# Kernel tuning notes

Hardware: AMD Instinct MI355X
Metric: run time of the kernel (lower is better)

Reference implementation:

```python
import jax, jax.numpy as jnp
import numpy as np

KSIZE = 20      # gaussian smoothing kernel size
SIGMA = 2.0     # gaussianSmoothWidth
STRIDE = 4      # strideLen
KLEN = 14       # kernelLen
LN_EPS = 1e-5


def _gauss_smooth(x):
    # x: [B, T, D]; depthwise conv1d along time, padding='same' (torch: left 9, right 10)
    D = x.shape[-1]
    i = jnp.arange(KSIZE, dtype=x.dtype)
    g = jnp.exp(-0.5 * ((i - (KSIZE - 1) / 2.0) / SIGMA) ** 2)
    g = g / jnp.sum(g)
    k = jnp.tile(g[None, None, :], (D, 1, 1))  # [D, 1, KSIZE]
    y = jax.lax.conv_general_dilated(
        jnp.swapaxes(x, 1, 2), k,
        window_strides=(1,), padding=[(9, 10)],
        feature_group_count=D,
        dimension_numbers=('NCW', 'OIW', 'NCW'))
    return jnp.swapaxes(y, 1, 2)


def _qrnn_layer(x, W, b):
    # SpeechBrain QuasiRNNLayer (output_gate=True, unidirectional, zoneout=0)
    # x: [B, T, F]; W: [3H, 2F]; b: [3H]
    xprev = jnp.concatenate([jnp.zeros_like(x[:, :1]), x[:, :-1]], axis=1)
    y = jnp.einsum('btf,gf->btg', jnp.concatenate([x, xprev], axis=-1), W) + b
    z, f, o = jnp.split(y, 3, axis=-1)
    z = jnp.tanh(z)
    f = jax.nn.sigmoid(f)
    fz = f * z
    # recurrence: c_t = f_t*z_t + (1-f_t)*c_{t-1}, c_0-input = 0
    def step(c, ins):
        f_t, fz_t = ins
        c = fz_t + (1.0 - f_t) * c
        return c, c
    c0 = jnp.zeros((f.shape[0], f.shape[2]), f.dtype)
    _, cs = jax.lax.scan(step, c0, (jnp.swapaxes(f, 0, 1), jnp.swapaxes(fz, 0, 1)))
    c = jnp.swapaxes(cs, 0, 1)  # [B, T, H]
    return jax.nn.sigmoid(o) * c


def reference(neuralInput, dayWeights, dayBias, w0, b0, w_rest, b_rest,
              ln_gamma, ln_beta, w_out, b_out, dayIdx):
    x = _gauss_smooth(neuralInput)                    # [B, T, D]
    Wd = dayWeights[dayIdx]                           # [B, D, D]
    bd = dayBias[dayIdx]                              # [B, 1, D]
    x = jnp.einsum('btd,bdk->btk', x, Wd) + bd
    x = x / (1.0 + jnp.abs(x))                        # Softsign
    B, T, D = x.shape
    Tp = (T - KLEN) // STRIDE + 1
    idx = jnp.arange(Tp)[:, None] * STRIDE + jnp.arange(KLEN)[None, :]
    win = x[:, idx, :]                                # [B, Tp, K, D]
    # torch Unfold ordering: channel-major -> feature index = d*KLEN + k
    strided = jnp.transpose(win, (0, 1, 3, 2)).reshape(B, Tp, D * KLEN)
    h = _qrnn_layer(strided, w0, b0)
    for i in range(w_rest.shape[0]):
        h = _qrnn_layer(h, w_rest[i], b_rest[i])
    mu = jnp.mean(h, axis=-1, keepdims=True)
    var = jnp.mean(jnp.square(h - mu), axis=-1, keepdims=True)
    hn = (h - mu) * jax.lax.rsqrt(var + LN_EPS) * ln_gamma + ln_beta
    return jnp.einsum('bth,ch->btc', hn, w_out) + b_out


def setup_inputs() -> dict:
    key = jax.random.key(0)
    ks = jax.random.split(key, 10)
    B, T, D, H, L, NDAYS, C = 32, 2000, 256, 512, 3, 24, 41
    F0 = D * KLEN  # 3584
    inp = {}
    inp['neuralInput'] = jax.random.normal(ks[0], (B, T, D), jnp.float32)
    inp['dayIdx'] = jax.random.randint(ks[1], (B,), 0, NDAYS, jnp.int64 if jax.config.jax_enable_x64 else jnp.int32)
    eye = jnp.eye(D, dtype=jnp.float32)
    inp['dayWeights'] = eye[None] + 0.02 * jax.random.normal(ks[2], (NDAYS, D, D), jnp.float32)
    inp['dayBias'] = jnp.zeros((NDAYS, 1, D), jnp.float32)
    inp['w0'] = jax.random.normal(ks[3], (3 * H, 2 * F0), jnp.float32) / np.sqrt(2 * F0)
    inp['b0'] = jnp.zeros((3 * H,), jnp.float32)
    inp['w_rest'] = jax.random.normal(ks[4], (L - 1, 3 * H, 2 * H), jnp.float32) / np.sqrt(2 * H)
    inp['b_rest'] = jnp.zeros((L - 1, 3 * H), jnp.float32)
    inp['ln_gamma'] = jnp.ones((H,), jnp.float32)
    inp['ln_beta'] = jnp.zeros((H,), jnp.float32)
    inp['w_out'] = jax.random.normal(ks[5], (C, H), jnp.float32) / np.sqrt(H)
    inp['b_out'] = jnp.zeros((C,), jnp.float32)
    return inp
```

## Files before the change

### kernel.cpp

```cpp
#include <hip/hip_runtime.h>
#include <hip/hip_bf16.h>

typedef __hip_bfloat16 bf16;
typedef __attribute__((ext_vector_type(8))) short bf16x8;
typedef __attribute__((ext_vector_type(4))) float f32x4;

__device__ __forceinline__ float fsig(float x) { return 1.f / (1.f + __expf(-x)); }
__device__ __forceinline__ float ftanh(float x) { return 1.f - 2.f / (1.f + __expf(2.f * x)); }

#define GT 16
__global__ __launch_bounds__(256) void gauss_kernel(const float* __restrict__ X,
                                                    bf16* __restrict__ Y, int T) {
  int b = blockIdx.y, t0 = blockIdx.x * GT;
  int tid = threadIdx.x;
  __shared__ float xs[GT + 19][256];
  const float* xb = X + (long)b * T * 256;
  for (int r = 0; r < GT + 19; ++r) {
    int tt = t0 + r - 9;
    xs[r][tid] = (tt >= 0 && tt < T) ? xb[(long)tt * 256 + tid] : 0.f;
  }
  __syncthreads();
  float g[20];
  float norm = 0.f;
#pragma unroll
  for (int j = 0; j < 20; ++j) {
    float u = (j - 9.5f) * 0.5f;
    g[j] = expf(-0.5f * u * u);
    norm += g[j];
  }
  float rn = 1.f / norm;
  for (int i = 0; i < GT; ++i) {
    int t = t0 + i;
    if (t >= T) break;
    float acc = 0.f;
#pragma unroll
    for (int j = 0; j < 20; ++j) acc += g[j] * xs[i + j][tid];
    Y[((long)b * T + t) * 256 + tid] = (bf16)(acc * rn);
  }
}

__global__ __launch_bounds__(256) void transpose_day(const float* __restrict__ W,
                                                     bf16* __restrict__ Wt) {
  __shared__ float tile[64][65];
  int d0 = blockIdx.x * 64, g0 = blockIdx.y * 64, day = blockIdx.z;
  const float* Wd = W + (long)day * 65536;
  int tx = threadIdx.x & 63, ty = threadIdx.x >> 6;
  for (int i = 0; i < 16; ++i) {
    int d = ty + i * 4;
    tile[d][tx] = Wd[(long)(d0 + d) * 256 + g0 + tx];
  }
  __syncthreads();
  bf16* outp = Wt + (((long)day * 4 + (d0 >> 6)) * 256 + g0) * 64;
  for (int i = 0; i < 16; ++i) {
    int g = ty + i * 4;
    outp[(long)g * 64 + tx] = (bf16)tile[tx][g];
  }
}

__global__ void prep_misc(const float* __restrict__ w0, const float* __restrict__ w_rest,
                          bf16* __restrict__ V2, bf16* __restrict__ wrb2,
                          bf16* __restrict__ w0b, bf16* __restrict__ h1s,
                          bf16* __restrict__ h2s, bf16* __restrict__ zpage) {
  long i = (long)blockIdx.x * 256 + threadIdx.x;
  if (i < 7077888L) {
    int u = (int)(i / (1536 * 256));
    int r = (int)(i % (1536 * 256));
    int g = r >> 8, d = r & 255;
    float v = 0.f;
    if (u < 14) v += w0[(long)g * 7168 + 3584 + d * 14 + u];
    if (u >= 4) v += w0[(long)g * 7168 + d * 14 + (u - 4)];
    V2[(((long)u * 4 + (d >> 6)) * 1536 + g) * 64 + (d & 63)] = (bf16)v;
    return;
  }
  i -= 7077888L;
  if (i < 3145728L) {
    int L = (int)(i / (1536 * 1024));
    int r = (int)(i % (1536 * 1024));
    int g = r >> 10, k = r & 1023;
    float v = w_rest[(long)L * 1536 * 1024 + (long)g * 1024 + (k ^ 512)];
    wrb2[(long)L * 16 * 1536 * 64 + ((long)(k >> 6) * 1536 + g) * 64 + (k & 63)] = (bf16)v;
    return;
  }
  i -= 3145728L;
  if (i < 5505024L) {
    long g = i / 3584;
    int j = (int)(i - g * 3584);
    w0b[i] = (bf16)w0[g * 7168 + j];
    return;
  }
  i -= 5505024L;
  if (i < 16384) {
    int b = (int)(i >> 9), k = (int)(i & 511);
    h1s[(long)b * 498 * 512 + k] = (bf16)0.f;
    h2s[(long)b * 498 * 512 + k] = (bf16)0.f;
    return;
  }
  i -= 16384;
  if (i < 128) zpage[i] = (bf16)0.f;
}

__global__ __launch_bounds__(256, 4) void mfma97(
    const bf16* __restrict__ A, const bf16* __restrict__ W,
    const float* __restrict__ bias, bf16* __restrict__ Y,
    const int* __restrict__ dayIdx, const bf16* __restrict__ zpage,
    long astride, int Ta, int rstride, int Tm, int N, int tstride,
    int ntaps, int nch, int tap_off0, int NW, long dayWStride,
    int dayBStride, int mode, int nti, int ngi) {
  __shared__ __align__(16) char smem[32768];
  const int id = blockIdx.x;
  const int bi = id / (ngi * nti);
  const int rem = id - bi * (ngi * nti);
  const int gi = rem / nti;
  const int ti = rem - gi * nti;
  const int g0 = gi * 128, t0 = ti * 128;

  const bf16* Ab = A + (long)bi * astride;
  long wbase = 0;
  int boff = 0;
  if (dayIdx) {
    int di = dayIdx[bi];
    wbase = (long)di * dayWStride;
    boff = di * dayBStride;
  }
  const int tid = threadIdx.x;
  const int lane = tid & 63;
  const int w = tid >> 6;
  const int wm = (w >> 1) * 64, wn = (w & 1) * 64;
  const int lr = lane & 15, lg = lane >> 4;

  f32x4 acc[4][4] = {};

  for (int tap = 0; tap < ntaps; ++tap) {
    for (int dblk = 0; dblk < nch; ++dblk) {
      int d0 = dblk << 6;
      int s = tap * nch + dblk;
      const bf16* Wp = W + wbase + ((long)s * NW + g0) * 64;
#pragma unroll
      for (int j = 0; j < 8; ++j) {
        int q = j * 256 + tid;
        int qw = j * 256 + w * 64;
        const bf16* src;
        if (j < 4) {
          int row = q >> 3;
          int u = (q & 7) ^ (row & 7);
          int time = (t0 + row) * tstride + tap + tap_off0;
          src = (time >= 0 && time < Ta) ? Ab + (long)time * rstride + d0 + u * 8
                                         : zpage;
        } else {
          int row = (q >> 3) - 128;
          int u = (q & 7) ^ (row & 7);
          src = Wp + row * 64 + u * 8;
        }
        auto lp = (__attribute__((address_space(3))) void*)(smem + qw * 16);
        __builtin_amdgcn_global_load_lds(
            (const __attribute__((address_space(1))) void*)src, lp, 16, 0, 0);
      }
      __syncthreads();
#pragma unroll
      for (int kc = 0; kc < 2; ++kc) {
        int ub = kc * 4 + lg;
        bf16x8 af[4], bw[4];
#pragma unroll
        for (int f = 0; f < 4; ++f) {
          int m = wm + f * 16 + lr;
          af[f] = *reinterpret_cast<const bf16x8*>(smem + m * 128 + ((ub ^ (m & 7)) << 4));
          int g = wn + f * 16 + lr;
          bw[f] = *reinterpret_cast<const bf16x8*>(smem + 16384 + g * 128 +
                                                   ((ub ^ (g & 7)) << 4));
        }
#pragma unroll
        for (int fm = 0; fm < 4; ++fm)
#pragma unroll
          for (int fn = 0; fn < 4; ++fn)
            acc[fm][fn] = __builtin_amdgcn_mfma_f32_16x16x32_bf16(af[fm], bw[fn],
                                                                  acc[fm][fn], 0, 0, 0);
      }
      __syncthreads();
    }
  }
#pragma unroll
  for (int fn = 0; fn < 4; ++fn) {
    int gcol = g0 + wn + fn * 16 + lr;
    float bb = bias[boff + gcol];
    int sect = gcol >> 9;
#pragma unroll
    for (int fm = 0; fm < 4; ++fm) {
#pragma unroll
      for (int rr = 0; rr < 4; ++rr) {
        int t = t0 + wm + fm * 16 + lg * 4 + rr;
        if (t >= Tm) continue;
        float v = acc[fm][fn][rr] + bb;
        float e;
        if (mode == 1) e = v / (1.f + fabsf(v));
        else e = (sect == 0) ? ftanh(v) : fsig(v);
        Y[((long)bi * Tm + t) * N + gcol] = (bf16)e;
      }
    }
  }
}

__global__ void build_A0(const bf16* __restrict__ xs, bf16* __restrict__ A0) {
  int idx = blockIdx.x * 256 + threadIdx.x;
  if (idx >= 32 * 3584) return;
  int b = idx / 3584, j = idx % 3584;
  int d = j / 14, u = j % 14;
  A0[idx] = xs[((long)b * 2000 + u) * 256 + d];
}

__global__ __launch_bounds__(256) void t0_gemm(const bf16* __restrict__ A0,
                                               const bf16* __restrict__ W0b,
                                               float* __restrict__ part) {
  int g0 = blockIdx.x * 128;
  int ks = blockIdx.y;
  int k0 = ks * 512;
  __shared__ __align__(16) bf16 Wl[128 * 64];
  __shared__ __align__(16) bf16 Alds[32 * 64];
  int tid = threadIdx.x;
  int lane = tid & 63, wave = tid >> 6;
  int wn = wave * 32;
  int lr = lane & 15, lg = lane >> 4;
  int srow = tid >> 3, su = tid & 7;
  f32x4 acc[2][2] = {};
  for (int c = 0; c < 8; ++c) {
    int d0 = k0 + c * 64;
#pragma unroll
    for (int i = 0; i < 4; ++i) {
      int m = srow + i * 32;
      *reinterpret_cast<bf16x8*>(&Wl[m * 64 + ((su ^ (m & 7)) << 3)]) =
          *reinterpret_cast<const bf16x8*>(W0b + (long)(g0 + m) * 3584 + d0 + su * 8);
    }
    {
      int m = srow;
      *reinterpret_cast<bf16x8*>(&Alds[m * 64 + ((su ^ (m & 7)) << 3)]) =
          *reinterpret_cast<const bf16x8*>(A0 + (long)m * 3584 + d0 + su * 8);
    }
    __syncthreads();
#pragma unroll
    for (int kc = 0; kc < 2; ++kc) {
      int ub = kc * 4 + lg;
      bf16x8 am[2], bw[2];
#pragma unroll
      for (int f = 0; f < 2; ++f) {
        int m = f * 16 + lr;
        am[f] = *reinterpret_cast<const bf16x8*>(&Alds[m * 64 + ((ub ^ (m & 7)) << 3)]);
        int g = wn + f * 16 + lr;
        bw[f] = *reinterpret_cast<const bf16x8*>(&Wl[g * 64 + ((ub ^ (g & 7)) << 3)]);
      }
#pragma unroll
      for (int fm = 0; fm < 2; ++fm)
#pragma unroll
        for (int fn = 0; fn < 2; ++fn)
          acc[fm][fn] = __builtin_amdgcn_mfma_f32_16x16x32_bf16(am[fm], bw[fn],
                                                                acc[fm][fn], 0, 0, 0);
    }
    __syncthreads();
  }
#pragma unroll
  for (int fn = 0; fn < 2; ++fn) {
    int gcol = g0 + wn + fn * 16 + lr;
#pragma unroll
    for (int fm = 0; fm < 2; ++fm)
#pragma unroll
      for (int r = 0; r < 4; ++r) {
        int brow = fm * 16 + lg * 4 + r;
        part[((long)ks * 32 + brow) * 1536 + gcol] = acc[fm][fn][r];
      }
  }
}

__global__ void t0_reduce(const float* __restrict__ part, const float* __restrict__ b0,
                          bf16* __restrict__ yact, int Tp) {
  int idx = blockIdx.x * 256 + threadIdx.x;
  if (idx >= 32 * 1536) return;
  int b = idx / 1536, g = idx % 1536;
  float s = b0[g];
#pragma unroll
  for (int k = 0; k < 7; ++k) s += part[((long)k * 32 + b) * 1536 + g];
  float e = (g < 512) ? ftanh(s) : fsig(s);
  yact[(long)b * Tp * 1536 + g] = (bf16)e;
}

#define NC 8
#define LC 63
__global__ __launch_bounds__(256) void scan_pass1(const bf16* __restrict__ Yv,
                                                  float* __restrict__ Afac,
                                                  float* __restrict__ Bfac, int Tp) {
  int idx = blockIdx.x * 256 + threadIdx.x;
  int ci = idx >> 14;
  int chain = idx & 16383;
  int b = chain >> 9, hh = chain & 511;
  const bf16* yb = Yv + (long)b * Tp * 1536 + hh;
  int t0 = ci * LC, t1 = min(t0 + LC, Tp);
  float A = 1.f, Bv = 0.f;
  for (int t = t0; t < t1; ++t) {
    const bf16* p = yb + (long)t * 1536;
    float zt = (float)p[0], fs = (float)p[512];
    Bv = fs * zt + (1.f - fs) * Bv;
    A *= (1.f - fs);
  }
  Afac[idx] = A;
  Bfac[idx] = Bv;
}

__global__ void scan_pass2(const float* __restrict__ Afac, const float* __restrict__ Bfac,
                           float* __restrict__ cst) {
  int chain = blockIdx.x * 256 + threadIdx.x;
  float c = 0.f;
#pragma unroll
  for (int ci = 0; ci < NC; ++ci) {
    cst[ci * 16384 + chain] = c;
    c = Afac[ci * 16384 + chain] * c + Bfac[ci * 16384 + chain];
  }
}

__global__ __launch_bounds__(256) void scan_pass3(const bf16* __restrict__ Yv,
                                                  const float* __restrict__ cst,
                                                  bf16* __restrict__ H, int Tp) {
  int idx = blockIdx.x * 256 + threadIdx.x;
  int ci = idx >> 14;
  int chain = idx & 16383;
  int b = chain >> 9, hh = chain & 511;
  const bf16* yb = Yv + (long)b * Tp * 1536 + hh;
  bf16* hb = H + ((long)b * 498 + 1) * 512 + hh;
  int t0 = ci * LC, t1 = min(t0 + LC, Tp);
  float c = cst[ci * 16384 + chain];
  for (int t = t0; t < t1; ++t) {
    const bf16* p = yb + (long)t * 1536;
    float zt = (float)p[0], fs = (float)p[512], so = (float)p[1024];
    c = fs * zt + (1.f - fs) * c;
    hb[(long)t * 512] = (bf16)(so * c);
  }
}

__global__ __launch_bounds__(256) void ln_out_kernel(
    const bf16* __restrict__ Hs, const float* __restrict__ gamma,
    const float* __restrict__ beta, const float* __restrict__ Wo,
    const float* __restrict__ bo, float* __restrict__ Out) {
  long bt = blockIdx.x;
  int b = (int)(bt / 497), t = (int)(bt % 497);
  const bf16* hrow = Hs + ((long)b * 498 + 1 + t) * 512;
  int tid = threadIdx.x;
  float v0 = (float)hrow[tid], v1 = (float)hrow[tid + 256];
  float s = v0 + v1, s2 = v0 * v0 + v1 * v1;
#pragma unroll
  for (int d = 32; d; d >>= 1) {
    s += __shfl_down(s, d);
    s2 += __shfl_down(s2, d);
  }
  __shared__ float rs[4], rs2[4];
  int wid = tid >> 6, lane = tid & 63;
  if (lane == 0) {
    rs[wid] = s;
    rs2[wid] = s2;
  }
  __syncthreads();
  float sum = rs[0] + rs[1] + rs[2] + rs[3];
  float sum2 = rs2[0] + rs2[1] + rs2[2] + rs2[3];
  float mu = sum * (1.f / 512.f);
  float var = sum2 * (1.f / 512.f) - mu * mu;
  float rstd = rsqrtf(var + 1e-5f);
  __shared__ float hl[512];
  hl[tid] = (v0 - mu) * rstd * gamma[tid] + beta[tid];
  hl[tid + 256] = (v1 - mu) * rstd * gamma[tid + 256] + beta[tid + 256];
  __syncthreads();
  const float4* hp = reinterpret_cast<const float4*>(&hl[lane * 8]);
  float4 h0v = hp[0], h1v = hp[1];
  for (int c = wid; c < 41; c += 4) {
    const float4* wp = reinterpret_cast<const float4*>(Wo + (long)c * 512 + lane * 8);
    float4 w0v = wp[0], w1v = wp[1];
    float a = w0v.x * h0v.x + w0v.y * h0v.y + w0v.z * h0v.z + w0v.w * h0v.w +
              w1v.x * h1v.x + w1v.y * h1v.y + w1v.z * h1v.z + w1v.w * h1v.w;
#pragma unroll
    for (int d = 32; d; d >>= 1) a += __shfl_down(a, d);
    if (lane == 0) Out[bt * 41 + c] = a + bo[c];
  }
}

extern "C" void kernel_launch(void* const* d_in, const int* in_sizes, int n_in,
                              void* d_out, int out_size, void* d_ws, size_t ws_size,
                              hipStream_t stream) {
  const float* neuralInput = (const float*)d_in[0];
  const int* dayIdx = (const int*)d_in[1];
  const float* dayWeights = (const float*)d_in[2];
  const float* dayBias = (const float*)d_in[3];
  const float* w0 = (const float*)d_in[4];
  const float* b0 = (const float*)d_in[5];
  const float* w_rest = (const float*)d_in[6];
  const float* b_rest = (const float*)d_in[7];
  const float* ln_gamma = (const float*)d_in[8];
  const float* ln_beta = (const float*)d_in[9];
  const float* w_out = (const float*)d_in[10];
  const float* b_out = (const float*)d_in[11];
  float* out = (float*)d_out;

  const int B = 32, T = 2000, Tp = 497;

  char* p = (char*)d_ws;
  bf16* yact = (bf16*)p;  p += 48857088;
  bf16* xs0b = (bf16*)p;  p += 32768000;
  bf16* xs = (bf16*)p;    p += 32768000;
  bf16* V2 = (bf16*)p;    p += 14155776;
  bf16* dWb2 = (bf16*)p;  p += 3145728;
  bf16* wrb2 = (bf16*)p;  p += 6291456;
  bf16* w0b = (bf16*)p;   p += 11010048;
  bf16* A0 = (bf16*)p;    p += 229376;
  float* part = (float*)p; p += 1376256;
  bf16* h1s = (bf16*)p;   p += 16320512;
  bf16* h2s = (bf16*)p;   p += 16320512;
  float* Afac = (float*)p; p += 524288;
  float* Bfac = (float*)p; p += 524288;
  float* cst = (float*)p;  p += 524288;
  bf16* zpage = (bf16*)p;  p += 256;

  hipLaunchKernelGGL(prep_misc, dim3((15745152L + 255) / 256), dim3(256), 0, stream,
                     w0, w_rest, V2, wrb2, w0b, h1s, h2s, zpage);
  hipLaunchKernelGGL(transpose_day, dim3(4, 4, 24), dim3(256), 0, stream, dayWeights, dWb2);
  hipLaunchKernelGGL(gauss_kernel, dim3((T + GT - 1) / GT, B), dim3(256), 0, stream,
                     neuralInput, xs0b, T);
  hipLaunchKernelGGL(mfma97, dim3(1024), dim3(256), 0, stream, xs0b, dWb2, dayBias,
                     xs, dayIdx, zpage, (long)T * 256, T, 256, T, 256, 1, 1, 4, 0,
                     256, 65536L, 256, 1, 16, 2);
  hipLaunchKernelGGL(build_A0, dim3((32 * 3584 + 255) / 256), dim3(256), 0, stream, xs, A0);
  hipLaunchKernelGGL(t0_gemm, dim3(12, 7), dim3(256), 0, stream, A0, w0b, part);
  hipLaunchKernelGGL(mfma97, dim3(1536), dim3(256), 0, stream, xs, V2, b0, yact,
                     (const int*)nullptr, zpage, (long)T * 256, T, 256, Tp, 1536, 4,
                     18, 4, -4, 1536, 0L, 0, 2, 4, 12);
  hipLaunchKernelGGL(t0_reduce, dim3((32 * 1536 + 255) / 256), dim3(256), 0, stream,
                     part, b0, yact, Tp);
  hipLaunchKernelGGL(scan_pass1, dim3(512), dim3(256), 0, stream, yact, Afac, Bfac, Tp);
  hipLaunchKernelGGL(scan_pass2, dim3(64), dim3(256), 0, stream, Afac, Bfac, cst);
  hipLaunchKernelGGL(scan_pass3, dim3(512), dim3(256), 0, stream, yact, cst, h1s, Tp);
  for (int i = 0; i < 2; ++i) {
    bf16* hin = (i == 0) ? h1s : h2s;
    bf16* hout = (i == 0) ? h2s : h1s;
    hipLaunchKernelGGL(mfma97, dim3(1536), dim3(256), 0, stream, hin,
                       wrb2 + (long)i * 16 * 1536 * 64, b_rest + (long)i * 1536, yact,
                       (const int*)nullptr, zpage, 498L * 512, Tp, 512, Tp, 1536, 1,
                       1, 16, 0, 1536, 0L, 0, 2, 4, 12);
    hipLaunchKernelGGL(scan_pass1, dim3(512), dim3(256), 0, stream, yact, Afac, Bfac, Tp);
    hipLaunchKernelGGL(scan_pass2, dim3(64), dim3(256), 0, stream, Afac, Bfac, cst);
    hipLaunchKernelGGL(scan_pass3, dim3(512), dim3(256), 0, stream, yact, cst, hout, Tp);
  }
  hipLaunchKernelGGL(ln_out_kernel, dim3(B * Tp), dim3(256), 0, stream, h1s,
                     ln_gamma, ln_beta, w_out, b_out, out);
}
```

Measured before the change: 816.9 us.

## Replace 128x128 GEMM with 256x256 8-wave ping-pong pipelined kernel

Result: slower. 982.0 us (+20.2%).

```diff
diff --git a/kernel.cpp b/kernel.cpp
--- a/kernel.cpp
+++ b/kernel.cpp
@@ -99,101 +99,145 @@
   if (i < 128) zpage[i] = (bf16)0.f;
 }
 
-__global__ __launch_bounds__(256, 4) void mfma97(
+#define MMAC(ACC)                                                                   \
+  __builtin_amdgcn_s_setprio(1);                                                    \
+  _Pragma("unroll") for (int fm = 0; fm < 4; ++fm)                                  \
+      _Pragma("unroll") for (int fn = 0; fn < 4; ++fn)                              \
+          ACC[fm][fn] = __builtin_amdgcn_mfma_f32_16x16x32_bf16(af[fm], bw[fn],     \
+                                                                ACC[fm][fn], 0, 0, 0); \
+  __builtin_amdgcn_s_setprio(0);
+#define BAR __builtin_amdgcn_s_barrier()
+
+__global__ __launch_bounds__(512, 1) void gemm8ph(
     const bf16* __restrict__ A, const bf16* __restrict__ W,
     const float* __restrict__ bias, bf16* __restrict__ Y,
     const int* __restrict__ dayIdx, const bf16* __restrict__ zpage,
     long astride, int Ta, int rstride, int Tm, int N, int tstride,
     int ntaps, int nch, int tap_off0, int NW, long dayWStride,
-    int dayBStride, int mode, int nti, int ngi) {
-  __shared__ __align__(16) char smem[32768];
-  const int id = blockIdx.x;
-  const int bi = id / (ngi * nti);
-  const int rem = id - bi * (ngi * nti);
-  const int gi = rem / nti;
-  const int ti = rem - gi * nti;
-  const int g0 = gi * 128, t0 = ti * 128;
-
-  const bf16* Ab = A + (long)bi * astride;
+    int dayBStride, int mode, int nti) {
+  extern __shared__ char smem[];
+  const int nwg = gridDim.x;
+  const int id = (blockIdx.x & 7) * (nwg >> 3) + (blockIdx.x >> 3);
+  const int b = id & 31;
+  const int rem = id >> 5;
+  const int ti = rem % nti, gi = rem / nti;
+  const int g0 = gi * 256, t0 = ti * 256;
+
+  const bf16* Ab = A + (long)b * astride;
   long wbase = 0;
   int boff = 0;
   if (dayIdx) {
-    int di = dayIdx[bi];
+    int di = dayIdx[b];
     wbase = (long)di * dayWStride;
     boff = di * dayBStride;
   }
   const int tid = threadIdx.x;
   const int lane = tid & 63;
   const int w = tid >> 6;
-  const int wm = (w >> 1) * 64, wn = (w & 1) * 64;
+  const int wr = w >> 2, wc = w & 3;
   const int lr = lane & 15, lg = lane >> 4;
-
-  f32x4 acc[4][4] = {};
-
-  for (int tap = 0; tap < ntaps; ++tap) {
-    for (int dblk = 0; dblk < nch; ++dblk) {
-      int d0 = dblk << 6;
-      int s = tap * nch + dblk;
-      const bf16* Wp = W + wbase + ((long)s * NW + g0) * 64;
-#pragma unroll
-      for (int j = 0; j < 8; ++j) {
-        int q = j * 256 + tid;
-        int qw = j * 256 + w * 64;
-        const bf16* src;
-        if (j < 4) {
-          int row = q >> 3;
-          int u = (q & 7) ^ (row & 7);
-          int time = (t0 + row) * tstride + tap + tap_off0;
-          src = (time >= 0 && time < Ta) ? Ab + (long)time * rstride + d0 + u * 8
-                                         : zpage;
-        } else {
-          int row = (q >> 3) - 128;
-          int u = (q & 7) ^ (row & 7);
-          src = Wp + row * 64 + u * 8;
-        }
-        auto lp = (__attribute__((address_space(3))) void*)(smem + qw * 16);
-        __builtin_amdgcn_global_load_lds(
-            (const __attribute__((address_space(1))) void*)src, lp, 16, 0, 0);
+  const int ns = ntaps * nch;
+  const int niter = ns >> 1;
+
+  auto stage = [&](int p, int op, int c, int kt) {
+    int tap = kt / nch;
+    int d0 = (kt - tap * nch) << 6;
+    int base = p * 65536 + op * 32768 + c * 16384;
+    const bf16* Wp = W + wbase + ((long)kt * NW + g0) * 64 + c * 32;
+#pragma unroll
+    for (int j = 0; j < 2; ++j) {
+      int q = j * 512 + tid;
+      int row = q >> 2, u = q & 3;
+      const bf16* src;
+      if (op == 0) {
+        int time = (t0 + row) * tstride + tap + tap_off0;
+        src = (time >= 0 && time < Ta)
+                  ? Ab + (long)time * rstride + d0 + c * 32 + u * 8
+                  : zpage;
+      } else {
+        src = Wp + (long)row * 64 + u * 8;
       }
-      __syncthreads();
-#pragma unroll
-      for (int kc = 0; kc < 2; ++kc) {
-        int ub = kc * 4 + lg;
-        bf16x8 af[4], bw[4];
-#pragma unroll
-        for (int f = 0; f < 4; ++f) {
-          int m = wm + f * 16 + lr;
-          af[f] = *reinterpret_cast<const bf16x8*>(smem + m * 128 + ((ub ^ (m & 7)) << 4));
-          int g = wn + f * 16 + lr;
-          bw[f] = *reinterpret_cast<const bf16x8*>(smem + 16384 + g * 128 +
-                                                   ((ub ^ (g & 7)) << 4));
-        }
-#pragma unroll
-        for (int fm = 0; fm < 4; ++fm)
-#pragma unroll
-          for (int fn = 0; fn < 4; ++fn)
-            acc[fm][fn] = __builtin_amdgcn_mfma_f32_16x16x32_bf16(af[fm], bw[fn],
-                                                                  acc[fm][fn], 0, 0, 0);
-      }
-      __syncthreads();
-    }
-  }
+      auto lp = (__attribute__((address_space(3))) void*)(smem + base + (j * 512 + w * 64) * 16);
+      __builtin_amdgcn_global_load_lds(
+          (const __attribute__((address_space(1))) void*)src, lp, 16, 0, 0);
+    }
+  };
+
+  f32x4 accL[4][4] = {};
+  f32x4 accH[4][4] = {};
+  bf16x8 af[4], bw[4];
+
+  auto rdA = [&](int p, int c, int mh) {
+#pragma unroll
+    for (int f = 0; f < 4; ++f) {
+      int m = wr * 128 + mh * 64 + f * 16 + lr;
+      af[f] = *reinterpret_cast<const bf16x8*>(smem + p * 65536 + c * 16384 + m * 64 + lg * 16);
+    }
+  };
+  auto rdB = [&](int p, int c) {
+#pragma unroll
+    for (int f = 0; f < 4; ++f) {
+      int g = wc * 64 + f * 16 + lr;
+      bw[f] = *reinterpret_cast<const bf16x8*>(smem + p * 65536 + 32768 + c * 16384 + g * 64 + lg * 16);
+    }
+  };
+
+  stage(0, 0, 0, 0); stage(0, 1, 0, 0);
+  stage(0, 0, 1, 0); stage(0, 1, 1, 0);
+  stage(1, 0, 0, 1); stage(1, 1, 0, 1);
+  asm volatile("s_waitcnt vmcnt(8)" ::: "memory");
+  BAR;
+
+  for (int i = 0; i < niter; ++i) {
+    const int k0 = 2 * i, k1 = 2 * i + 1;
+    const bool more = (i + 1 < niter);
+    rdB(0, 0); rdA(0, 0, 0); stage(1, 0, 1, k1);
+    BAR; MMAC(accL); BAR;
+    rdA(0, 0, 1); stage(1, 1, 1, k1);
+    BAR; MMAC(accH);
+    if (more) { asm volatile("s_waitcnt vmcnt(8)" ::: "memory"); }
+    else      { asm volatile("s_waitcnt vmcnt(0)" ::: "memory"); }
+    BAR;
+    rdB(0, 1); rdA(0, 1, 0); if (more) stage(0, 0, 0, k0 + 2);
+    BAR; MMAC(accL); BAR;
+    rdA(0, 1, 1); if (more) stage(0, 1, 0, k0 + 2);
+    BAR; MMAC(accH);
+    if (more) { asm volatile("s_waitcnt vmcnt(8)" ::: "memory"); }
+    else      { asm volatile("s_waitcnt vmcnt(0)" ::: "memory"); }
+    BAR;
+    rdB(1, 0); rdA(1, 0, 0); if (more) stage(0, 0, 1, k0 + 2);
+    BAR; MMAC(accL); BAR;
+    rdA(1, 0, 1); if (more) stage(0, 1, 1, k0 + 2);
+    BAR; MMAC(accH);
+    if (more) { asm volatile("s_waitcnt vmcnt(8)" ::: "memory"); }
+    else      { asm volatile("s_waitcnt vmcnt(0)" ::: "memory"); }
+    BAR;
+    rdB(1, 1); rdA(1, 1, 0); if (more) stage(1, 0, 0, k1 + 2);
+    BAR; MMAC(accL); BAR;
+    rdA(1, 1, 1); if (more) stage(1, 1, 0, k1 + 2);
+    BAR; MMAC(accH);
+    if (more) { asm volatile("s_waitcnt vmcnt(8)" ::: "memory"); }
+    else      { asm volatile("s_waitcnt vmcnt(0)" ::: "memory"); }
+    BAR;
+  }
+
 #pragma unroll
   for (int fn = 0; fn < 4; ++fn) {
-    int gcol = g0 + wn + fn * 16 + lr;
+    int gcol = g0 + wc * 64 + fn * 16 + lr;
     float bb = bias[boff + gcol];
     int sect = gcol >> 9;
 #pragma unroll
-    for (int fm = 0; fm < 4; ++fm) {
+    for (int fm = 0; fm < 8; ++fm) {
+      f32x4 a = (fm < 4) ? accL[fm][fn] : accH[fm - 4][fn];
 #pragma unroll
       for (int rr = 0; rr < 4; ++rr) {
-        int t = t0 + wm + fm * 16 + lg * 4 + rr;
+        int t = t0 + wr * 128 + fm * 16 + lg * 4 + rr;
         if (t >= Tm) continue;
-        float v = acc[fm][fn][rr] + bb;
+        float v = a[rr] + bb;
         float e;
         if (mode == 1) e = v / (1.f + fabsf(v));
         else e = (sect == 0) ? ftanh(v) : fsig(v);
-        Y[((long)bi * Tm + t) * N + gcol] = (bf16)e;
+        Y[((long)b * Tm + t) * N + gcol] = (bf16)e;
       }
     }
   }
@@ -238,19 +282,19 @@
 #pragma unroll
     for (int kc = 0; kc < 2; ++kc) {
       int ub = kc * 4 + lg;
-      bf16x8 am[2], bw[2];
+      bf16x8 am[2], bwv[2];
 #pragma unroll
       for (int f = 0; f < 2; ++f) {
         int m = f * 16 + lr;
         am[f] = *reinterpret_cast<const bf16x8*>(&Alds[m * 64 + ((ub ^ (m & 7)) << 3)]);
         int g = wn + f * 16 + lr;
-        bw[f] = *reinterpret_cast<const bf16x8*>(&Wl[g * 64 + ((ub ^ (g & 7)) << 3)]);
+        bwv[f] = *reinterpret_cast<const bf16x8*>(&Wl[g * 64 + ((ub ^ (g & 7)) << 3)]);
       }
 #pragma unroll
       for (int fm = 0; fm < 2; ++fm)
 #pragma unroll
         for (int fn = 0; fn < 2; ++fn)
-          acc[fm][fn] = __builtin_amdgcn_mfma_f32_16x16x32_bf16(am[fm], bw[fn],
+          acc[fm][fn] = __builtin_amdgcn_mfma_f32_16x16x32_bf16(am[fm], bwv[fn],
                                                                 acc[fm][fn], 0, 0, 0);
     }
     __syncthreads();
@@ -412,19 +456,23 @@
   float* cst = (float*)p;  p += 524288;
   bf16* zpage = (bf16*)p;  p += 256;
 
+  const int LDS8 = 131072;
+  hipFuncSetAttribute(reinterpret_cast<const void*>(gemm8ph),
+                      hipFuncAttributeMaxDynamicSharedMemorySize, LDS8);
+
   hipLaunchKernelGGL(prep_misc, dim3((15745152L + 255) / 256), dim3(256), 0, stream,
                      w0, w_rest, V2, wrb2, w0b, h1s, h2s, zpage);
   hipLaunchKernelGGL(transpose_day, dim3(4, 4, 24), dim3(256), 0, stream, dayWeights, dWb2);
   hipLaunchKernelGGL(gauss_kernel, dim3((T + GT - 1) / GT, B), dim3(256), 0, stream,
                      neuralInput, xs0b, T);
-  hipLaunchKernelGGL(mfma97, dim3(1024), dim3(256), 0, stream, xs0b, dWb2, dayBias,
+  hipLaunchKernelGGL(gemm8ph, dim3(256), dim3(512), LDS8, stream, xs0b, dWb2, dayBias,
                      xs, dayIdx, zpage, (long)T * 256, T, 256, T, 256, 1, 1, 4, 0,
-                     256, 65536L, 256, 1, 16, 2);
+                     256, 65536L, 256, 1, 8);
   hipLaunchKernelGGL(build_A0, dim3((32 * 3584 + 255) / 256), dim3(256), 0, stream, xs, A0);
   hipLaunchKernelGGL(t0_gemm, dim3(12, 7), dim3(256), 0, stream, A0, w0b, part);
-  hipLaunchKernelGGL(mfma97, dim3(1536), dim3(256), 0, stream, xs, V2, b0, yact,
+  hipLaunchKernelGGL(gemm8ph, dim3(384), dim3(512), LDS8, stream, xs, V2, b0, yact,
                      (const int*)nullptr, zpage, (long)T * 256, T, 256, Tp, 1536, 4,
-                     18, 4, -4, 1536, 0L, 0, 2, 4, 12);
+                     18, 4, -4, 1536, 0L, 0, 2, 2);
   hipLaunchKernelGGL(t0_reduce, dim3((32 * 1536 + 255) / 256), dim3(256), 0, stream,
                      part, b0, yact, Tp);
   hipLaunchKernelGGL(scan_pass1, dim3(512), dim3(256), 0, stream, yact, Afac, Bfac, Tp);
@@ -433,10 +481,10 @@
   for (int i = 0; i < 2; ++i) {
     bf16* hin = (i == 0) ? h1s : h2s;
     bf16* hout = (i == 0) ? h2s : h1s;
-    hipLaunchKernelGGL(mfma97, dim3(1536), dim3(256), 0, stream, hin,
+    hipLaunchKernelGGL(gemm8ph, dim3(384), dim3(512), LDS8, stream, hin,
                        wrb2 + (long)i * 16 * 1536 * 64, b_rest + (long)i * 1536, yact,
                        (const int*)nullptr, zpage, 498L * 512, Tp, 512, Tp, 1536, 1,
-                       1, 16, 0, 1536, 0L, 0, 2, 4, 12);
+                       1, 16, 0, 1536, 0L, 0, 2, 2);
     hipLaunchKernelGGL(scan_pass1, dim3(512), dim3(256), 0, stream, yact, Afac, Bfac, Tp);
     hipLaunchKernelGGL(scan_pass2, dim3(64), dim3(256), 0, stream, Afac, Bfac, cst);
     hipLaunchKernelGGL(scan_pass3, dim3(512), dim3(256), 0, stream, yact, cst, hout, Tp);
```

## Add 256x256 ping-pong GEMM with direct-to-LDS loads and fold scan pass2 into pass3

Applied to the files above, without the earlier changes.

Measured after the change: 992.5 us. 21.5% more time.

```diff
diff --git a/kernel.cpp b/kernel.cpp
--- a/kernel.cpp
+++ b/kernel.cpp
@@ -97,6 +97,138 @@
   }
   i -= 16384;
   if (i < 128) zpage[i] = (bf16)0.f;
+}
+
+#define MM16(MH)                                                                     \
+  __builtin_amdgcn_s_setprio(1);                                                     \
+  _Pragma("unroll") for (int fm = 0; fm < 4; ++fm)                                   \
+      _Pragma("unroll") for (int fn = 0; fn < 4; ++fn)                               \
+          acc[MH][fm][fn] = __builtin_amdgcn_mfma_f32_16x16x32_bf16(                 \
+              af[fm], bw[fn], acc[MH][fm][fn], 0, 0, 0);                             \
+  __builtin_amdgcn_s_setprio(0);
+#define BAR __builtin_amdgcn_s_barrier()
+
+__global__ __launch_bounds__(512, 1) void gemm8p2(
+    const bf16* __restrict__ A, const bf16* __restrict__ W,
+    const float* __restrict__ bias, bf16* __restrict__ Y,
+    const bf16* __restrict__ zpage, long astride, int Ta, int rstride,
+    int Tm, int N, int tstride, int ntaps, int nch, int tap_off0, int NW,
+    int nti) {
+  extern __shared__ char smem[];
+  const int nwg = gridDim.x;
+  const int id = (blockIdx.x & 7) * (nwg >> 3) + (blockIdx.x >> 3);
+  const int ngi = N >> 8;
+  const int per_b = ngi * nti;
+  const int b = id / per_b;
+  const int rem = id - b * per_b;
+  const int gi = rem / nti, ti = rem - (rem / nti) * nti;
+  const int g0 = gi * 256, t0 = ti * 256;
+
+  const bf16* Ab = A + (long)b * astride;
+  const int tid = threadIdx.x;
+  const int lane = tid & 63;
+  const int w = tid >> 6;
+  const int wr = w >> 2, wc = w & 3;
+  const int lr = lane & 15, lg = lane >> 4;
+  const int ns = ntaps * nch;
+  const int niter = ns >> 1;
+
+  auto st = [&](int p, int op, int h, int kt) {
+    int tap = kt / nch;
+    int d0 = (kt - tap * nch) << 6;
+    int base = p * 65536 + op * 32768 + h * 16384;
+#pragma unroll
+    for (int j = 0; j < 2; ++j) {
+      int q = j * 512 + tid;
+      int row = h * 128 + (q >> 3);
+      int u = (q & 7) ^ (row & 7);
+      const bf16* src;
+      if (op == 0) {
+        int time = (t0 + row) * tstride + tap + tap_off0;
+        src = (time >= 0 && time < Ta) ? Ab + (long)time * rstride + d0 + u * 8
+                                       : zpage;
+      } else {
+        src = W + ((long)kt * NW + g0 + row) * 64 + u * 8;
+      }
+      auto lp = (__attribute__((address_space(3))) void*)(smem + base + (j * 512 + w * 64) * 16);
+      __builtin_amdgcn_global_load_lds(
+          (const __attribute__((address_space(1))) void*)src, lp, 16, 0, 0);
+    }
+  };
+
+  f32x4 acc[2][4][4] = {};
+  bf16x8 af[4], bw[4];
+
+  auto rdA = [&](int p, int c, int mh) {
+#pragma unroll
+    for (int f = 0; f < 4; ++f) {
+      int m = wr * 128 + mh * 64 + f * 16 + lr;
+      af[f] = *reinterpret_cast<const bf16x8*>(
+          smem + p * 65536 + m * 128 + (((c * 4 + lg) ^ (m & 7)) << 4));
+    }
+  };
+  auto rdB = [&](int p, int c) {
+#pragma unroll
+    for (int f = 0; f < 4; ++f) {
+      int g = wc * 64 + f * 16 + lr;
+      bw[f] = *reinterpret_cast<const bf16x8*>(
+          smem + p * 65536 + 32768 + g * 128 + (((c * 4 + lg) ^ (g & 7)) << 4));
+    }
+  };
+
+  st(0, 0, 0, 0); st(0, 0, 1, 0); st(0, 1, 0, 0); st(0, 1, 1, 0);
+  st(1, 0, 0, 1);
+  asm volatile("s_waitcnt vmcnt(2)" ::: "memory");
+  BAR;
+
+#pragma unroll 1
+  for (int i = 0; i < niter; ++i) {
+    const int k0 = 2 * i, k1 = 2 * i + 1;
+    const bool more = (i + 1 < niter);
+    rdA(0, 0, 0); rdB(0, 0); st(1, 0, 1, k1);
+    BAR; MM16(0); BAR;
+    rdA(0, 0, 1); st(1, 1, 0, k1);
+    BAR; MM16(1); BAR;
+    rdA(0, 1, 0); rdB(0, 1); st(1, 1, 1, k1);
+    BAR; MM16(0); BAR;
+    rdA(0, 1, 1); if (more) st(0, 0, 0, k0 + 2);
+    BAR; MM16(1);
+    if (more) { asm volatile("s_waitcnt vmcnt(2)" ::: "memory"); }
+    else      { asm volatile("s_waitcnt vmcnt(0)" ::: "memory"); }
+    BAR;
+    rdA(1, 0, 0); rdB(1, 0); if (more) st(0, 0, 1, k0 + 2);
+    BAR; MM16(0); BAR;
+    rdA(1, 0, 1); if (more) st(0, 1, 0, k0 + 2);
+    BAR; MM16(1); BAR;
+    rdA(1, 1, 0); rdB(1, 1); if (more) st(0, 1, 1, k0 + 2);
+    BAR; MM16(0); BAR;
+    rdA(1, 1, 1); if (more) st(1, 0, 0, k1 + 2);
+    BAR; MM16(1);
+    if (more) { asm volatile("s_waitcnt vmcnt(2)" ::: "memory"); }
+    else      { asm volatile("s_waitcnt vmcnt(0)" ::: "memory"); }
+    BAR;
+  }
+
+#pragma unroll
+  for (int fn = 0; fn < 4; ++fn) {
+    int gcol = g0 + wc * 64 + fn * 16 + lr;
+    float bb = bias[gcol];
+    int sect = gcol >> 9;
+#pragma unroll
+    for (int mh = 0; mh < 2; ++mh) {
+#pragma unroll
+      for (int fm = 0; fm < 4; ++fm) {
+#pragma unroll
+        for (int rr = 0; rr < 4; ++rr) {
+          int t = t0 + wr * 128 + mh * 64 + fm * 16 + lg * 4 + rr;
+          if (t >= Tm) continue;
+          float v = acc[mh][fm][fn][rr] + bb;
+          float e = (sect == 0) ? ftanh(v) : fsig(v);
+          Y[((long)b * Tm + t) * N + gcol] = (bf16)e;
+        }
+      }
+    }
+  }
 }
 
 __global__ __launch_bounds__(256, 4) void mfma97(
@@ -238,19 +370,19 @@
 #pragma unroll
     for (int kc = 0; kc < 2; ++kc) {
       int ub = kc * 4 + lg;
-      bf16x8 am[2], bw[2];
+      bf16x8 am[2], bwv[2];
 #pragma unroll
       for (int f = 0; f < 2; ++f) {
         int m = f * 16 + lr;
         am[f] = *reinterpret_cast<const bf16x8*>(&Alds[m * 64 + ((ub ^ (m & 7)) << 3)]);
         int g = wn + f * 16 + lr;
-        bw[f] = *reinterpret_cast<const bf16x8*>(&Wl[g * 64 + ((ub ^ (g & 7)) << 3)]);
+        bwv[f] = *reinterpret_cast<const bf16x8*>(&Wl[g * 64 + ((ub ^ (g & 7)) << 3)]);
       }
 #pragma unroll
       for (int fm = 0; fm < 2; ++fm)
 #pragma unroll
         for (int fn = 0; fn < 2; ++fn)
-          acc[fm][fn] = __builtin_amdgcn_mfma_f32_16x16x32_bf16(am[fm], bw[fn],
+          acc[fm][fn] = __builtin_amdgcn_mfma_f32_16x16x32_bf16(am[fm], bwv[fn],
                                                                 acc[fm][fn], 0, 0, 0);
     }
     __syncthreads();
@@ -302,19 +434,9 @@
   Bfac[idx] = Bv;
 }
 
-__global__ void scan_pass2(const float* __restrict__ Afac, const float* __restrict__ Bfac,
-                           float* __restrict__ cst) {
-  int chain = blockIdx.x * 256 + threadIdx.x;
-  float c = 0.f;
-#pragma unroll
-  for (int ci = 0; ci < NC; ++ci) {
-    cst[ci * 16384 + chain] = c;
-    c = Afac[ci * 16384 + chain] * c + Bfac[ci * 16384 + chain];
-  }
-}
-
 __global__ __launch_bounds__(256) void scan_pass3(const bf16* __restrict__ Yv,
-                                                  const float* __restrict__ cst,
+                                                  const float* __restrict__ Afac,
+                                                  const float* __restrict__ Bfac,
                                                   bf16* __restrict__ H, int Tp) {
   int idx = blockIdx.x * 256 + threadIdx.x;
   int ci = idx >> 14;
@@ -322,8 +444,10 @@
   int b = chain >> 9, hh = chain & 511;
   const bf16* yb = Yv + (long)b * Tp * 1536 + hh;
   bf16* hb = H + ((long)b * 498 + 1) * 512 + hh;
+  float c = 0.f;
+  for (int k = 0; k < ci; ++k)
+    c = Afac[k * 16384 + chain] * c + Bfac[k * 16384 + chain];
   int t0 = ci * LC, t1 = min(t0 + LC, Tp);
-  float c = cst[ci * 16384 + chain];
   for (int t = t0; t < t1; ++t) {
     const bf16* p = yb + (long)t * 1536;
     float zt = (float)p[0], fs = (float)p[512], so = (float)p[1024];
@@ -409,8 +533,11 @@
   bf16* h2s = (bf16*)p;   p += 16320512;
   float* Afac = (float*)p; p += 524288;
   float* Bfac = (float*)p; p += 524288;
-  float* cst = (float*)p;  p += 524288;
   bf16* zpage = (bf16*)p;  p += 256;
+
+  const int LDS8 = 131072;
+  hipFuncSetAttribute(reinterpret_cast<const void*>(gemm8p2),
+                      hipFuncAttributeMaxDynamicSharedMemorySize, LDS8);
 
   hipLaunchKernelGGL(prep_misc, dim3((15745152L + 255) / 256), dim3(256), 0, stream,
                      w0, w_rest, V2, wrb2, w0b, h1s, h2s, zpage);
@@ -422,24 +549,20 @@
                      256, 65536L, 256, 1, 16, 2);
   hipLaunchKernelGGL(build_A0, dim3((32 * 3584 + 255) / 256), dim3(256), 0, stream, xs, A0);
   hipLaunchKernelGGL(t0_gemm, dim3(12, 7), dim3(256), 0, stream, A0, w0b, part);
-  hipLaunchKernelGGL(mfma97, dim3(1536), dim3(256), 0, stream, xs, V2, b0, yact,
-                     (const int*)nullptr, zpage, (long)T * 256, T, 256, Tp, 1536, 4,
-                     18, 4, -4, 1536, 0L, 0, 2, 4, 12);
+  hipLaunchKernelGGL(gemm8p2, dim3(384), dim3(512), LDS8, stream, xs, V2, b0, yact,
+                     zpage, (long)T * 256, T, 256, Tp, 1536, 4, 18, 4, -4, 1536, 2);
   hipLaunchKernelGGL(t0_reduce, dim3((32 * 1536 + 255) / 256), dim3(256), 0, stream,
                      part, b0, yact, Tp);
   hipLaunchKernelGGL(scan_pass1, dim3(512), dim3(256), 0, stream, yact, Afac, Bfac, Tp);
-  hipLaunchKernelGGL(scan_pass2, dim3(64), dim3(256), 0, stream, Afac, Bfac, cst);
-  hipLaunchKernelGGL(scan_pass3, dim3(512), dim3(256), 0, stream, yact, cst, h1s, Tp);
+  hipLaunchKernelGGL(scan_pass3, dim3(512), dim3(256), 0, stream, yact, Afac, Bfac, h1s, Tp);
   for (int i = 0; i < 2; ++i) {
     bf16* hin = (i == 0) ? h1s : h2s;
     bf16* hout = (i == 0) ? h2s : h1s;
-    hipLaunchKernelGGL(mfma97, dim3(1536), dim3(256), 0, stream, hin,
+    hipLaunchKernelGGL(gemm8p2, dim3(384), dim3(512), LDS8, stream, hin,
                        wrb2 + (long)i * 16 * 1536 * 64, b_rest + (long)i * 1536, yact,
-                       (const int*)nullptr, zpage, 498L * 512, Tp, 512, Tp, 1536, 1,
-                       1, 16, 0, 1536, 0L, 0, 2, 4, 12);
+                       zpage, 498L * 512, Tp, 512, Tp, 1536, 1, 1, 16, 0, 1536, 2);
     hipLaunchKernelGGL(scan_pass1, dim3(512), dim3(256), 0, stream, yact, Afac, Bfac, Tp);
-    hipLaunchKernelGGL(scan_pass2, dim3(64), dim3(256), 0, stream, Afac, Bfac, cst);
-    hipLaunchKernelGGL(scan_pass3, dim3(512), dim3(256), 0, stream, yact, cst, hout, Tp);
+    hipLaunchKernelGGL(scan_pass3, dim3(512), dim3(256), 0, stream, yact, Afac, Bfac, hout, Tp);
   }
   hipLaunchKernelGGL(ln_out_kernel, dim3(B * Tp), dim3(256), 0, stream, h1s,
                      ln_gamma, ln_beta, w_out, b_out, out);
```
